# Kernel tuning notes

Measured on AMD Instinct MI355X. Metric: run time of the kernel, lower is better.

## Reference

```python
import jax, jax.numpy as jnp
import numpy as np

HEAD_SIZE = 128  # embeddings_dims // no_of_heads = 4096 // 32


def apply_rope(v):
    # v: [B, S, d] with d = HEAD_SIZE; interleaved-pair rotation as in source
    B, S, d = v.shape
    pos = jnp.arange(S, dtype=jnp.float32)[:, None]              # [S, 1]
    idx = jnp.arange(0, d, 2, dtype=jnp.float32)[None, :]        # [1, d//2]
    theta = jnp.power(10000.0, -2.0 * idx / d)                   # [1, d//2]
    angles = pos * theta                                         # [S, d//2]
    cos = jnp.cos(angles)
    sin = jnp.sin(angles)
    vr = v.reshape(B, S, d // 2, 2)
    x0, x1 = vr[..., 0], vr[..., 1]
    out = jnp.stack([x0 * cos - x1 * sin, x1 * cos + x0 * sin], axis=-1)
    return out.reshape(B, S, d)


def setup_inputs() -> dict:
    key = jax.random.key(0)
    kx, kq, kk, kv = jax.random.split(key, 4)
    B, S, D = 2, 4096, 4096
    d = HEAD_SIZE
    scale = 1.0 / np.sqrt(D)
    return {
        "x": jax.random.normal(kx, (B, S, D), dtype=jnp.float32),
        "Wq": jax.random.normal(kq, (d, D), dtype=jnp.float32) * scale,
        "Wk": jax.random.normal(kk, (d, D), dtype=jnp.float32) * scale,
        "Wv": jax.random.normal(kv, (d, D), dtype=jnp.float32) * scale,
    }


def reference(x, Wq, Wk, Wv):
    # single attention head, non-flash path (eval mode: dropout = identity)
    B, S, D = x.shape
    q = jnp.einsum('bsd,hd->bsh', x, Wq)  # [B, S, head]
    k = jnp.einsum('bsd,hd->bsh', x, Wk)
    v = jnp.einsum('bsd,hd->bsh', x, Wv)
    q = apply_rope(q)
    k = apply_rope(k)
    scale = k.shape[-1] ** (-0.5)
    scores = jnp.einsum('bqh,bkh->bqk', q, k) * scale  # [B, S, S]
    causal = jnp.tril(jnp.ones((S, S), dtype=bool))
    scores = jnp.where(causal, scores, -jnp.inf)
    weights = jax.nn.softmax(scores, axis=-1)
    out = jnp.einsum('bqk,bkh->bqh', weights, v)  # [B, S, head]
    return out
```

## Files before the change

kernel.cpp:

```cpp
#include <hip/hip_runtime.h>

typedef _Float16 half8 __attribute__((ext_vector_type(8)));
typedef _Float16 half2v __attribute__((ext_vector_type(2)));
typedef float f32x4 __attribute__((ext_vector_type(4)));

#define S_LEN 4096
#define D_DIM 4096
#define HD 128


__device__ __forceinline__ void gload_lds16(const _Float16* g, _Float16* l) {
    __builtin_amdgcn_global_load_lds(
        (const __attribute__((address_space(1))) unsigned int*)g,
        (__attribute__((address_space(3))) unsigned int*)l, 16, 0, 0);
}

__global__ __launch_bounds__(256) void convw_kernel(const float* __restrict__ wq,
                                                    const float* __restrict__ wk,
                                                    const float* __restrict__ wv,
                                                    _Float16* __restrict__ wh) {
    const int g = blockIdx.x * 256 + threadIdx.x;
    const int p = g >> 16;
    const int off = (g & 65535) * 8;
    const float* src = ((p == 0) ? wq : (p == 1) ? wk : wv) + off;
    float4 v0 = *(const float4*)src;
    float4 v1 = *(const float4*)(src + 4);
    half8 h = { (_Float16)v0.x, (_Float16)v0.y, (_Float16)v0.z, (_Float16)v0.w,
                (_Float16)v1.x, (_Float16)v1.y, (_Float16)v1.z, (_Float16)v1.w };
    *(half8*)&wh[(size_t)p * 524288 + off] = h;
}

__global__ __launch_bounds__(256) void trig_kernel(float* __restrict__ tab) {
    const int g = blockIdx.x * 256 + threadIdx.x;
    const int s = g >> 6, p = g & 63;
    const float theta = exp2f((float)p * -0.4152410118609203f);
    float sn, cn;
    sincosf((float)s * theta, &sn, &cn);
    *(float2*)&tab[g * 2] = (float2){cn, sn};
}

__global__ __launch_bounds__(256, 3) void proj64_kernel(const float* __restrict__ x,
                                                        const _Float16* __restrict__ wh,
                                                        float* __restrict__ P) {
    __shared__ __align__(16) _Float16 smem[24576];
    const int tid = threadIdx.x;
    const int wg = blockIdx.x;
    const int swz = (wg & 7) * 96 + (wg >> 3);
    const int bx = swz % 3;
    const int rest = swz / 3;
    const int ks = rest & 1;
    const int M0 = (rest >> 1) * 64;
    const int lane = tid & 63, wv_ = tid >> 6;
    const int l15 = lane & 15, quad = lane >> 4;

    const int arow = tid >> 2, acol = (tid & 3) * 16;
    const float* xa = x + (size_t)(M0 + arow) * D_DIM + acol + ks * (D_DIM / 2);
    const int c8a = (tid & 3) * 2;
    const int awoff0 = (((arow >> 4) * 2 + (c8a >> 2)) * 64 + (arow & 15) + (c8a & 3) * 16) * 8;
    const int c8b = c8a + 1;
    const int awoff1 = (((arow >> 4) * 2 + (c8b >> 2)) * 64 + (arow & 15) + (c8b & 3) * 16) * 8;

    const _Float16* wsrc = wh + (size_t)bx * 524288 + ks * (D_DIM / 2) +
                           (size_t)(wv_ * 32 + l15) * D_DIM + quad * 8;

    f32x4 acc[4][2];
    for (int mi = 0; mi < 4; ++mi)
        for (int ni = 0; ni < 2; ++ni)
            acc[mi][ni] = (f32x4){0.f, 0.f, 0.f, 0.f};

    auto stageA = [&](_Float16* buf, float4 A0, float4 A1, float4 A2, float4 A3) {
        half8 h0 = { (_Float16)A0.x, (_Float16)A0.y, (_Float16)A0.z, (_Float16)A0.w,
                     (_Float16)A1.x, (_Float16)A1.y, (_Float16)A1.z, (_Float16)A1.w };
        half8 h1 = { (_Float16)A2.x, (_Float16)A2.y, (_Float16)A2.z, (_Float16)A2.w,
                     (_Float16)A3.x, (_Float16)A3.y, (_Float16)A3.z, (_Float16)A3.w };
        *(half8*)&buf[awoff0] = h0;
        *(half8*)&buf[awoff1] = h1;
    };
    auto stageB = [&](_Float16* buf, int p) {
        const _Float16* s = wsrc + p * 64;
        gload_lds16(s,                     &buf[4096 + ((wv_ * 2 + 0) * 2 + 0) * 512]);
        gload_lds16(s + 32,                &buf[4096 + ((wv_ * 2 + 0) * 2 + 1) * 512]);
        gload_lds16(s + 16 * D_DIM,        &buf[4096 + ((wv_ * 2 + 1) * 2 + 0) * 512]);
        gload_lds16(s + 16 * D_DIM + 32,   &buf[4096 + ((wv_ * 2 + 1) * 2 + 1) * 512]);
    };
    auto compute = [&](const _Float16* buf) {
        const _Float16* Af = buf + lane * 8;
        const _Float16* Bf = buf + 4096 + wv_ * 2048 + lane * 8;
        half8 af[4][2], bf[2][2];
        for (int mi = 0; mi < 4; ++mi)
            for (int kk = 0; kk < 2; ++kk)
                af[mi][kk] = *(const half8*)(Af + (mi * 2 + kk) * 512);
        for (int ni = 0; ni < 2; ++ni)
            for (int kk = 0; kk < 2; ++kk)
                bf[ni][kk] = *(const half8*)(Bf + (ni * 2 + kk) * 512);
        for (int kk = 0; kk < 2; ++kk)
            for (int mi = 0; mi < 4; ++mi)
                for (int ni = 0; ni < 2; ++ni)
                    acc[mi][ni] = __builtin_amdgcn_mfma_f32_16x16x32_f16(af[mi][kk], bf[ni][kk],
                                                                         acc[mi][ni], 0, 0, 0);
    };

#define LOADA(R0, R1, R2, R3, p)                           \
    R0 = *(const float4*)(xa + (p) * 64);                  \
    R1 = *(const float4*)(xa + (p) * 64 + 4);              \
    R2 = *(const float4*)(xa + (p) * 64 + 8);              \
    R3 = *(const float4*)(xa + (p) * 64 + 12);

    float4 aA0, aA1, aA2, aA3, aB0, aB1, aB2, aB3;
    LOADA(aA0, aA1, aA2, aA3, 0)
    LOADA(aB0, aB1, aB2, aB3, 1)
    stageB(smem, 0);

    for (int p = 0; p < 32; p += 2) {
        stageA(smem, aA0, aA1, aA2, aA3);
        __syncthreads();
        if (p + 2 < 32) { LOADA(aA0, aA1, aA2, aA3, p + 2) }
        stageB(smem + 12288, p + 1);
        compute(smem);
        stageA(smem + 12288, aB0, aB1, aB2, aB3);
        __syncthreads();
        if (p + 3 < 32) { LOADA(aB0, aB1, aB2, aB3, p + 3) }
        if (p + 2 < 32) stageB(smem, p + 2);
        compute(smem + 12288);
    }
#undef LOADA
    __syncthreads();

    float* sf = (float*)smem;
    for (int mi = 0; mi < 4; ++mi)
        for (int ni = 0; ni < 2; ++ni)
            for (int r = 0; r < 4; ++r)
                sf[(mi * 16 + quad * 4 + r) * 132 + wv_ * 32 + ni * 16 + l15] =
                    acc[mi][ni][r];
    __syncthreads();
    const int row = tid >> 2, c0 = (tid & 3) * 32;
    float* dst = P + ((size_t)(ks * 3 + bx) * 8192 + M0 + row) * HD + c0;
    for (int j = 0; j < 8; ++j)
        *(float4*)(dst + j * 4) = *(const float4*)&sf[row * 132 + c0 + j * 4];
}

#define QSTR 136
__global__ __launch_bounds__(256) void proj_kernel(const float* __restrict__ x,
                                                   const _Float16* __restrict__ wh,
                                                   _Float16* __restrict__ qw,
                                                   _Float16* __restrict__ kw,
                                                   _Float16* __restrict__ vt) {
    __shared__ __align__(16) _Float16 smem[17408];
    const int tid = threadIdx.x;
    const int wg = blockIdx.x;
    const int swz = (wg & 7) * 48 + (wg >> 3);
    const int bx = swz % 3;
    const int M0 = (swz / 3) * 64;
    const int lane = tid & 63, wv_ = tid >> 6;
    const int l15 = lane & 15, quad = lane >> 4;

    const int arow = tid >> 2, acol = (tid & 3) * 8;
    const float* xa = x + (size_t)(M0 + arow) * D_DIM + acol;
    const _Float16* wsrc = wh + (size_t)bx * 128 * D_DIM +
                           (size_t)(wv_ * 32 + l15) * D_DIM + quad * 8;
    const int awoff = ((arow >> 4) * 64 + (arow & 15) + (tid & 3) * 16) * 8;
    const int rdoff = lane * 8;

    f32x4 acc[4][2];
    for (int mi = 0; mi < 4; ++mi)
        for (int ni = 0; ni < 2; ++ni)
            acc[mi][ni] = (f32x4){0.f, 0.f, 0.f, 0.f};

    auto stageA = [&](_Float16* buf, float4 A0, float4 A1) {
        half8 ha = { (_Float16)A0.x, (_Float16)A0.y, (_Float16)A0.z, (_Float16)A0.w,
                     (_Float16)A1.x, (_Float16)A1.y, (_Float16)A1.z, (_Float16)A1.w };
        *(half8*)&buf[awoff] = ha;
    };
    auto stageB = [&](_Float16* buf, int slab) {
        const _Float16* s = wsrc + slab * 32;
        gload_lds16(s,              &buf[2048 + wv_ * 1024]);
        gload_lds16(s + 16 * D_DIM, &buf[2048 + wv_ * 1024 + 512]);
    };
    auto compute = [&](const _Float16* buf) {
        const _Float16* Af = buf + rdoff;
        const _Float16* Bf = buf + 2048 + wv_ * 1024 + rdoff;
        half8 af[4], bf[2];
        for (int mi = 0; mi < 4; ++mi)
            af[mi] = *(const half8*)(Af + mi * 512);
        for (int ni = 0; ni < 2; ++ni)
            bf[ni] = *(const half8*)(Bf + ni * 512);
        for (int mi = 0; mi < 4; ++mi)
            for (int ni = 0; ni < 2; ++ni)
                acc[mi][ni] = __builtin_amdgcn_mfma_f32_16x16x32_f16(af[mi], bf[ni],
                                                                     acc[mi][ni], 0, 0, 0);
    };

    float4 a0_0, a0_1, a1_0, a1_1;
    a0_0 = *(const float4*)(xa);      a0_1 = *(const float4*)(xa + 4);
    a1_0 = *(const float4*)(xa + 32); a1_1 = *(const float4*)(xa + 36);
    stageB(smem, 0);

    for (int i = 0; i < 128; i += 2) {
        stageA(smem, a0_0, a0_1);
        __syncthreads();
        if (i + 2 < 128) {
            a0_0 = *(const float4*)(xa + (i + 2) * 32);
            a0_1 = *(const float4*)(xa + (i + 2) * 32 + 4);
        }
        stageB(smem + 6144, i + 1);
        compute(smem);
        stageA(smem + 6144, a1_0, a1_1);
        __syncthreads();
        if (i + 3 < 128) {
            a1_0 = *(const float4*)(xa + (i + 3) * 32);
            a1_1 = *(const float4*)(xa + (i + 3) * 32 + 4);
        }
        if (i + 2 < 128) stageB(smem, i + 2);
        compute(smem + 6144);
    }
    __syncthreads();

    if (bx < 2) {
        for (int mi = 0; mi < 4; ++mi)
            for (int ni = 0; ni < 2; ++ni)
                for (int r = 0; r < 4; ++r)
                    smem[(mi * 16 + quad * 4 + r) * QSTR + wv_ * 32 + ni * 16 + l15] =
                        (_Float16)acc[mi][ni][r];
        __syncthreads();
        _Float16* dst = ((bx == 0) ? qw : kw) + (size_t)M0 * HD;
        const int row = tid >> 2, c0 = (tid & 3) * 32;
        for (int j = 0; j < 4; ++j)
            *(half8*)&dst[row * HD + c0 + j * 8] = *(const half8*)&smem[row * QSTR + c0 + j * 8];
    } else {
        for (int mi = 0; mi < 4; ++mi)
            for (int ni = 0; ni < 2; ++ni)
                for (int r = 0; r < 4; ++r)
                    smem[(wv_ * 32 + ni * 16 + l15) * QSTR + mi * 16 + quad * 4 + r] =
                        (_Float16)acc[mi][ni][r];
        __syncthreads();
        _Float16* dst = vt + (size_t)(M0 >> 12) * HD * S_LEN + (M0 & (S_LEN - 1));
        const int hd = tid >> 1, s0 = (tid & 1) * 32;
        for (int j = 0; j < 4; ++j)
            *(half8*)&dst[(size_t)hd * S_LEN + s0 + j * 8] =
                *(const half8*)&smem[hd * QSTR + s0 + j * 8];
    }
}

__global__ __launch_bounds__(256) void combine_kernel(const float* __restrict__ P,
                                                      const float* __restrict__ tab,
                                                      _Float16* __restrict__ qw,
                                                      _Float16* __restrict__ kw,
                                                      _Float16* __restrict__ vt) {
    const int tid = threadIdx.x;
    const int M0 = blockIdx.x * 64;
    const int row = tid >> 2, c0 = (tid & 3) * 32;
    if (blockIdx.y == 0) {
        const float* Pq0 = P + ((size_t)0 * 8192 + M0 + row) * HD + c0;
        const float* Pq1 = P + ((size_t)3 * 8192 + M0 + row) * HD + c0;
        const float* Pk0 = P + ((size_t)1 * 8192 + M0 + row) * HD + c0;
        const float* Pk1 = P + ((size_t)4 * 8192 + M0 + row) * HD + c0;
        float qv[32], kv[32];
#pragma unroll
        for (int j = 0; j < 8; ++j) {
            float4 a = *(const float4*)(Pq0 + j * 4);
            float4 b = *(const float4*)(Pq1 + j * 4);
            float4 c = *(const float4*)(Pk0 + j * 4);
            float4 d = *(const float4*)(Pk1 + j * 4);
            qv[j * 4 + 0] = a.x + b.x; qv[j * 4 + 1] = a.y + b.y;
            qv[j * 4 + 2] = a.z + b.z; qv[j * 4 + 3] = a.w + b.w;
            kv[j * 4 + 0] = c.x + d.x; kv[j * 4 + 1] = c.y + d.y;
            kv[j * 4 + 2] = c.z + d.z; kv[j * 4 + 3] = c.w + d.w;
        }
        const int s = (M0 + row) & (S_LEN - 1);
        const float2* tb = (const float2*)tab + s * 64 + (c0 >> 1);
        half8 oq[4], ok[4];
#pragma unroll
        for (int jp = 0; jp < 16; ++jp) {
            const float2 cs = tb[jp];
            const float cn = cs.x, sn = cs.y;
            const float q0 = qv[2 * jp], q1 = qv[2 * jp + 1];
            const float k0 = kv[2 * jp], k1 = kv[2 * jp + 1];
            oq[jp >> 2][(2 * jp) & 7]     = (_Float16)(q0 * cn - q1 * sn);
            oq[jp >> 2][(2 * jp + 1) & 7] = (_Float16)(q1 * cn + q0 * sn);
            ok[jp >> 2][(2 * jp) & 7]     = (_Float16)(k0 * cn - k1 * sn);
            ok[jp >> 2][(2 * jp + 1) & 7] = (_Float16)(k1 * cn + k0 * sn);
        }
        _Float16* qdst = qw + (size_t)(M0 + row) * HD + c0;
        _Float16* kdst = kw + (size_t)(M0 + row) * HD + c0;
#pragma unroll
        for (int j = 0; j < 4; ++j) {
            *(half8*)(qdst + j * 8) = oq[j];
            *(half8*)(kdst + j * 8) = ok[j];
        }
    } else {
        __shared__ __align__(16) _Float16 sh[128][72];
        const float* Pv0 = P + ((size_t)2 * 8192 + M0 + row) * HD + c0;
        const float* Pv1 = P + ((size_t)5 * 8192 + M0 + row) * HD + c0;
#pragma unroll
        for (int j = 0; j < 8; ++j) {
            float4 a = *(const float4*)(Pv0 + j * 4);
            float4 b = *(const float4*)(Pv1 + j * 4);
            sh[c0 + j * 4 + 0][row] = (_Float16)(a.x + b.x);
            sh[c0 + j * 4 + 1][row] = (_Float16)(a.y + b.y);
            sh[c0 + j * 4 + 2][row] = (_Float16)(a.z + b.z);
            sh[c0 + j * 4 + 3][row] = (_Float16)(a.w + b.w);
        }
        __syncthreads();
        const int hd = tid >> 1, s0 = (tid & 1) * 32;
        _Float16* dst = vt + (size_t)(M0 >> 12) * HD * S_LEN + (size_t)hd * S_LEN +
                        (M0 & (S_LEN - 1)) + s0;
        for (int j = 0; j < 4; ++j)
            *(half8*)(dst + j * 8) = *(const half8*)&sh[hd][s0 + j * 8];
    }
}

__global__ __launch_bounds__(256) void rope_kernel(_Float16* __restrict__ qw,
                                                   _Float16* __restrict__ kw) {
    const int g = blockIdx.x * 256 + threadIdx.x;
    const int m = g >> 6, p = g & 63;
    const int s = m & (S_LEN - 1);
    const float theta = exp2f((float)p * -0.4152410118609203f);
    float sn, cn;
    sincosf((float)s * theta, &sn, &cn);
    const size_t off = (size_t)m * HD + 2 * p;
    half2v qv = *(half2v*)&qw[off];
    half2v kv = *(half2v*)&kw[off];
    float q0 = qv[0], q1 = qv[1], k0 = kv[0], k1 = kv[1];
    half2v qo = { (_Float16)(q0 * cn - q1 * sn), (_Float16)(q1 * cn + q0 * sn) };
    half2v ko = { (_Float16)(k0 * cn - k1 * sn), (_Float16)(k1 * cn + k0 * sn) };
    *(half2v*)&qw[off] = qo;
    *(half2v*)&kw[off] = ko;
}

__device__ __forceinline__ void load_kf(const _Float16* __restrict__ kb, int kbase,
                                        int l15, int quad, half8* kf) {
    const _Float16* kr = kb + (size_t)(kbase + l15) * HD + quad * 8;
    for (int kk = 0; kk < 4; ++kk) {
        kf[kk]     = *(const half8*)(kr + kk * 32);
        kf[4 + kk] = *(const half8*)(kr + 16 * HD + kk * 32);
    }
}

template<bool MASKED>
__device__ __forceinline__ void attn_tile(int kbase, int qg, int l15, int quad,
                                          const half8* kf,
                                          const _Float16* __restrict__ vtb,
                                          const half8* bq, f32x4* acc,
                                          float& mrun, float& lrun) {
    const float csc = 0.1275174348796053f;
    half8 va[8];
    const _Float16* vr = vtb + (size_t)l15 * S_LEN + kbase + quad * 8;
    for (int c = 0; c < 8; ++c)
        va[c] = *(const half8*)(vr + (size_t)c * 16 * S_LEN);
    f32x4 st0 = (f32x4){0.f, 0.f, 0.f, 0.f};
    f32x4 st1 = (f32x4){0.f, 0.f, 0.f, 0.f};
    for (int kk = 0; kk < 4; ++kk) {
        st0 = __builtin_amdgcn_mfma_f32_16x16x32_f16(kf[kk],     bq[kk], st0, 0, 0, 0);
        st1 = __builtin_amdgcn_mfma_f32_16x16x32_f16(kf[4 + kk], bq[kk], st1, 0, 0, 0);
    }
    float p0[4], p1[4];
    float mloc = -1e30f;
    for (int r = 0; r < 4; ++r) {
        float v0 = st0[r] * csc;
        float v1 = st1[r] * csc;
        if (MASKED) {
            const int key0 = kbase + quad * 4 + r;
            if (key0 > qg)      v0 = -1e30f;
            if (key0 + 16 > qg) v1 = -1e30f;
        }
        p0[r] = v0; p1[r] = v1;
        mloc = fmaxf(mloc, fmaxf(v0, v1));
    }
    mloc = fmaxf(mloc, __shfl_xor(mloc, 16));
    mloc = fmaxf(mloc, __shfl_xor(mloc, 32));
    const float mnew = fmaxf(mrun, mloc);
    const float alpha = exp2f(mrun - mnew);
    mrun = mnew;
    float ls = 0.f;
    for (int r = 0; r < 4; ++r) {
        p0[r] = exp2f(p0[r] - mnew);
        p1[r] = exp2f(p1[r] - mnew);
        ls += p0[r] + p1[r];
    }
    ls += __shfl_xor(ls, 16);
    ls += __shfl_xor(ls, 32);
    lrun = lrun * alpha + ls;
    for (int c = 0; c < 8; ++c)
        acc[c] *= alpha;
    int ph0 = __builtin_bit_cast(int, __builtin_amdgcn_cvt_pkrtz(p0[0], p0[1]));
    int ph1 = __builtin_bit_cast(int, __builtin_amdgcn_cvt_pkrtz(p0[2], p0[3]));
    int ph2 = __builtin_bit_cast(int, __builtin_amdgcn_cvt_pkrtz(p1[0], p1[1]));
    int ph3 = __builtin_bit_cast(int, __builtin_amdgcn_cvt_pkrtz(p1[2], p1[3]));
    const int s0 = (l15 + (((quad << 1)    ) & 3) * 16) * 4;
    const int s1 = (l15 + (((quad << 1) + 1) & 3) * 16) * 4;
    int a0 = __builtin_amdgcn_ds_bpermute(s0, ph0);
    int a1 = __builtin_amdgcn_ds_bpermute(s0, ph1);
    int a2 = __builtin_amdgcn_ds_bpermute(s1, ph0);
    int a3 = __builtin_amdgcn_ds_bpermute(s1, ph1);
    int b0 = __builtin_amdgcn_ds_bpermute(s0, ph2);
    int b1 = __builtin_amdgcn_ds_bpermute(s0, ph3);
    int b2 = __builtin_amdgcn_ds_bpermute(s1, ph2);
    int b3 = __builtin_amdgcn_ds_bpermute(s1, ph3);
    const bool lo = quad < 2;
    int4 pi = { lo ? a0 : b0, lo ? a1 : b1, lo ? a2 : b2, lo ? a3 : b3 };
    half8 pf = __builtin_bit_cast(half8, pi);
    for (int c = 0; c < 8; ++c)
        acc[c] = __builtin_amdgcn_mfma_f32_16x16x32_f16(va[c], pf, acc[c], 0, 0, 0);
}

__global__ __launch_bounds__(256) void attn_kernel(const _Float16* __restrict__ q,
                                                   const _Float16* __restrict__ k,
                                                   const _Float16* __restrict__ vt,
                                                   float* __restrict__ out) {
    __shared__ __align__(16) float Osh[4][16][132];
    __shared__ float msh[4][16];
    __shared__ float lsh[4][16];
    const int tid = threadIdx.x;
    const int lane = tid & 63, wv_ = tid >> 6;
    const int l15 = lane & 15, quad = lane >> 4;
    const int bidx = blockIdx.x;
    const int b = bidx & 1;
    const int t = 255 - (bidx >> 1);
    const int qb = t * 16;
    const int qg = qb + l15;

    const _Float16* qp = q + (size_t)(b * S_LEN + qb) * HD;
    half8 bq[4];
    for (int kk = 0; kk < 4; ++kk)
        bq[kk] = *(const half8*)&qp[l15 * HD + kk * 32 + quad * 8];

    f32x4 acc[8];
    for (int c = 0; c < 8; ++c) acc[c] = (f32x4){0.f, 0.f, 0.f, 0.f};
    float mrun = -1e30f, lrun = 0.f;

    const _Float16* kb = k + (size_t)b * S_LEN * HD;
    const _Float16* vtb = vt + (size_t)b * HD * S_LEN;

    const int nfull = (qb + 1) >> 5;
    const int kend = nfull * 32;
    const bool hasm = ((nfull & 3) == wv_);
    const int kb0 = wv_ * 32;

    half8 kf[8], kf2[8];
    if (kb0 < kend)      load_kf(kb, kb0, l15, quad, kf);
    else if (hasm)       load_kf(kb, kend, l15, quad, kf);
    for (int kbase = kb0; kbase < kend; kbase += 128) {
        const int kn = kbase + 128;
        if (kn < kend)   load_kf(kb, kn, l15, quad, kf2);
        else if (hasm)   load_kf(kb, kend, l15, quad, kf2);
        attn_tile<false>(kbase, qg, l15, quad, kf, vtb, bq, acc, mrun, lrun);
        for (int j = 0; j < 8; ++j) kf[j] = kf2[j];
    }
    if (hasm)
        attn_tile<true>(kend, qg, l15, quad, kf, vtb, bq, acc, mrun, lrun);

    for (int c = 0; c < 8; ++c)
        *(f32x4*)&Osh[wv_][l15][c * 16 + quad * 4] = acc[c];
    if (quad == 0) { msh[wv_][l15] = mrun; lsh[wv_][l15] = lrun; }
    __syncthreads();

    const int qr = tid >> 4, dg = (tid & 15) * 8;
    float m0 = msh[0][qr], m1 = msh[1][qr], m2 = msh[2][qr], m3 = msh[3][qr];
    float mm = fmaxf(fmaxf(m0, m1), fmaxf(m2, m3));
    float f0 = exp2f(m0 - mm), f1 = exp2f(m1 - mm), f2 = exp2f(m2 - mm), f3 = exp2f(m3 - mm);
    float l = lsh[0][qr] * f0 + lsh[1][qr] * f1 + lsh[2][qr] * f2 + lsh[3][qr] * f3;
    f32x4 oa = (f32x4){0.f, 0.f, 0.f, 0.f}, ob = oa;
    oa += *(f32x4*)&Osh[0][qr][dg] * f0;  ob += *(f32x4*)&Osh[0][qr][dg + 4] * f0;
    oa += *(f32x4*)&Osh[1][qr][dg] * f1;  ob += *(f32x4*)&Osh[1][qr][dg + 4] * f1;
    oa += *(f32x4*)&Osh[2][qr][dg] * f2;  ob += *(f32x4*)&Osh[2][qr][dg + 4] * f2;
    oa += *(f32x4*)&Osh[3][qr][dg] * f3;  ob += *(f32x4*)&Osh[3][qr][dg + 4] * f3;
    const float inv = 1.0f / l;
    float* op = out + (size_t)(b * S_LEN + qb + qr) * HD + dg;
    *(float4*)op       = (float4){oa[0] * inv, oa[1] * inv, oa[2] * inv, oa[3] * inv};
    *(float4*)(op + 4) = (float4){ob[0] * inv, ob[1] * inv, ob[2] * inv, ob[3] * inv};
}

extern "C" void kernel_launch(void* const* d_in, const int* in_sizes, int n_in,
                              void* d_out, int out_size, void* d_ws, size_t ws_size,
                              hipStream_t stream) {
    const float* x  = (const float*)d_in[0];
    const float* Wq = (const float*)d_in[1];
    const float* Wk = (const float*)d_in[2];
    const float* Wv = (const float*)d_in[3];
    float* out = (float*)d_out;
    char* ws = (char*)d_ws;
    _Float16* qw = (_Float16*)(ws);
    _Float16* kw = (_Float16*)(ws + (2u << 20));
    _Float16* vt = (_Float16*)(ws + (4u << 20));
    _Float16* wh = (_Float16*)(ws + (6u << 20));
    float* P   = (float*)(ws + (9u << 20));
    float* tab = (float*)(ws + (33u << 20));

    const size_t need = (size_t)(35u << 20);
    convw_kernel<<<dim3(768), dim3(256), 0, stream>>>(Wq, Wk, Wv, wh);
    if (ws_size >= need) {
        trig_kernel<<<dim3(1024), dim3(256), 0, stream>>>(tab);
        proj64_kernel<<<dim3(768), dim3(256), 0, stream>>>(x, wh, P);
        combine_kernel<<<dim3(128, 2), dim3(256), 0, stream>>>(P, tab, qw, kw, vt);
    } else {
        proj_kernel<<<dim3(384), dim3(256), 0, stream>>>(x, wh, qw, kw, vt);
        rope_kernel<<<dim3(2048), dim3(256), 0, stream>>>(qw, kw);
    }
    attn_kernel<<<dim3(512), dim3(256), 0, stream>>>(qw, kw, vt, out);
}
```

Before: 349.5 us.

## Process 32 query rows per attention block, fuse setup kernels, drop fallback path

The attention kernel now handles two 16-row query sub-tiles per block. Each K and V tile is loaded once and reused for both, which halves the grid to 256 blocks, and the K double-buffer prefetch is removed. The weight-conversion and trig-table kernels are merged into one launch, and the small-workspace fallback path is deleted. The aim is to cut K/V global traffic and launch overhead, at the cost of more registers, lower occupancy, a smaller grid with coarser causal load balance, and no prefetch overlap.

```diff
diff --git a/kernel.cpp b/kernel.cpp
--- a/kernel.cpp
+++ b/kernel.cpp
@@ -15,28 +15,29 @@
         (__attribute__((address_space(3))) unsigned int*)l, 16, 0, 0);
 }
 
-__global__ __launch_bounds__(256) void convw_kernel(const float* __restrict__ wq,
+__global__ __launch_bounds__(256) void setup_kernel(const float* __restrict__ wq,
                                                     const float* __restrict__ wk,
                                                     const float* __restrict__ wv,
-                                                    _Float16* __restrict__ wh) {
+                                                    _Float16* __restrict__ wh,
+                                                    float* __restrict__ tab) {
     const int g = blockIdx.x * 256 + threadIdx.x;
-    const int p = g >> 16;
-    const int off = (g & 65535) * 8;
-    const float* src = ((p == 0) ? wq : (p == 1) ? wk : wv) + off;
-    float4 v0 = *(const float4*)src;
-    float4 v1 = *(const float4*)(src + 4);
-    half8 h = { (_Float16)v0.x, (_Float16)v0.y, (_Float16)v0.z, (_Float16)v0.w,
-                (_Float16)v1.x, (_Float16)v1.y, (_Float16)v1.z, (_Float16)v1.w };
-    *(half8*)&wh[(size_t)p * 524288 + off] = h;
-}
-
-__global__ __launch_bounds__(256) void trig_kernel(float* __restrict__ tab) {
-    const int g = blockIdx.x * 256 + threadIdx.x;
-    const int s = g >> 6, p = g & 63;
-    const float theta = exp2f((float)p * -0.4152410118609203f);
-    float sn, cn;
-    sincosf((float)s * theta, &sn, &cn);
-    *(float2*)&tab[g * 2] = (float2){cn, sn};
+    if (g < 196608) {
+        const int p = g >> 16;
+        const int off = (g & 65535) * 8;
+        const float* src = ((p == 0) ? wq : (p == 1) ? wk : wv) + off;
+        float4 v0 = *(const float4*)src;
+        float4 v1 = *(const float4*)(src + 4);
+        half8 h = { (_Float16)v0.x, (_Float16)v0.y, (_Float16)v0.z, (_Float16)v0.w,
+                    (_Float16)v1.x, (_Float16)v1.y, (_Float16)v1.z, (_Float16)v1.w };
+        *(half8*)&wh[(size_t)p * 524288 + off] = h;
+    } else {
+        const int h = g - 196608;
+        const int s = h >> 6, p = h & 63;
+        const float theta = exp2f((float)p * -0.4152410118609203f);
+        float sn, cn;
+        sincosf((float)s * theta, &sn, &cn);
+        *(float2*)&tab[h * 2] = (float2){cn, sn};
+    }
 }
 
 __global__ __launch_bounds__(256, 3) void proj64_kernel(const float* __restrict__ x,
@@ -78,10 +79,10 @@
     };
     auto stageB = [&](_Float16* buf, int p) {
         const _Float16* s = wsrc + p * 64;
-        gload_lds16(s,                     &buf[4096 + ((wv_ * 2 + 0) * 2 + 0) * 512]);
-        gload_lds16(s + 32,                &buf[4096 + ((wv_ * 2 + 0) * 2 + 1) * 512]);
-        gload_lds16(s + 16 * D_DIM,        &buf[4096 + ((wv_ * 2 + 1) * 2 + 0) * 512]);
-        gload_lds16(s + 16 * D_DIM + 32,   &buf[4096 + ((wv_ * 2 + 1) * 2 + 1) * 512]);
+        gload_lds16(s,                   &buf[4096 + ((wv_ * 2 + 0) * 2 + 0) * 512]);
+        gload_lds16(s + 32,              &buf[4096 + ((wv_ * 2 + 0) * 2 + 1) * 512]);
+        gload_lds16(s + 16 * D_DIM,      &buf[4096 + ((wv_ * 2 + 1) * 2 + 0) * 512]);
+        gload_lds16(s + 16 * D_DIM + 32, &buf[4096 + ((wv_ * 2 + 1) * 2 + 1) * 512]);
     };
     auto compute = [&](const _Float16* buf) {
         const _Float16* Af = buf + lane * 8;
@@ -137,108 +138,6 @@
     float* dst = P + ((size_t)(ks * 3 + bx) * 8192 + M0 + row) * HD + c0;
     for (int j = 0; j < 8; ++j)
         *(float4*)(dst + j * 4) = *(const float4*)&sf[row * 132 + c0 + j * 4];
-}
-
-#define QSTR 136
-__global__ __launch_bounds__(256) void proj_kernel(const float* __restrict__ x,
-                                                   const _Float16* __restrict__ wh,
-                                                   _Float16* __restrict__ qw,
-                                                   _Float16* __restrict__ kw,
-                                                   _Float16* __restrict__ vt) {
-    __shared__ __align__(16) _Float16 smem[17408];
-    const int tid = threadIdx.x;
-    const int wg = blockIdx.x;
-    const int swz = (wg & 7) * 48 + (wg >> 3);
-    const int bx = swz % 3;
-    const int M0 = (swz / 3) * 64;
-    const int lane = tid & 63, wv_ = tid >> 6;
-    const int l15 = lane & 15, quad = lane >> 4;
-
-    const int arow = tid >> 2, acol = (tid & 3) * 8;
-    const float* xa = x + (size_t)(M0 + arow) * D_DIM + acol;
-    const _Float16* wsrc = wh + (size_t)bx * 128 * D_DIM +
-                           (size_t)(wv_ * 32 + l15) * D_DIM + quad * 8;
-    const int awoff = ((arow >> 4) * 64 + (arow & 15) + (tid & 3) * 16) * 8;
-    const int rdoff = lane * 8;
-
-    f32x4 acc[4][2];
-    for (int mi = 0; mi < 4; ++mi)
-        for (int ni = 0; ni < 2; ++ni)
-            acc[mi][ni] = (f32x4){0.f, 0.f, 0.f, 0.f};
-
-    auto stageA = [&](_Float16* buf, float4 A0, float4 A1) {
-        half8 ha = { (_Float16)A0.x, (_Float16)A0.y, (_Float16)A0.z, (_Float16)A0.w,
-                     (_Float16)A1.x, (_Float16)A1.y, (_Float16)A1.z, (_Float16)A1.w };
-        *(half8*)&buf[awoff] = ha;
-    };
-    auto stageB = [&](_Float16* buf, int slab) {
-        const _Float16* s = wsrc + slab * 32;
-        gload_lds16(s,              &buf[2048 + wv_ * 1024]);
-        gload_lds16(s + 16 * D_DIM, &buf[2048 + wv_ * 1024 + 512]);
-    };
-    auto compute = [&](const _Float16* buf) {
-        const _Float16* Af = buf + rdoff;
-        const _Float16* Bf = buf + 2048 + wv_ * 1024 + rdoff;
-        half8 af[4], bf[2];
-        for (int mi = 0; mi < 4; ++mi)
-            af[mi] = *(const half8*)(Af + mi * 512);
-        for (int ni = 0; ni < 2; ++ni)
-            bf[ni] = *(const half8*)(Bf + ni * 512);
-        for (int mi = 0; mi < 4; ++mi)
-            for (int ni = 0; ni < 2; ++ni)
-                acc[mi][ni] = __builtin_amdgcn_mfma_f32_16x16x32_f16(af[mi], bf[ni],
-                                                                     acc[mi][ni], 0, 0, 0);
-    };
-
-    float4 a0_0, a0_1, a1_0, a1_1;
-    a0_0 = *(const float4*)(xa);      a0_1 = *(const float4*)(xa + 4);
-    a1_0 = *(const float4*)(xa + 32); a1_1 = *(const float4*)(xa + 36);
-    stageB(smem, 0);
-
-    for (int i = 0; i < 128; i += 2) {
-        stageA(smem, a0_0, a0_1);
-        __syncthreads();
-        if (i + 2 < 128) {
-            a0_0 = *(const float4*)(xa + (i + 2) * 32);
-            a0_1 = *(const float4*)(xa + (i + 2) * 32 + 4);
-        }
-        stageB(smem + 6144, i + 1);
-        compute(smem);
-        stageA(smem + 6144, a1_0, a1_1);
-        __syncthreads();
-        if (i + 3 < 128) {
-            a1_0 = *(const float4*)(xa + (i + 3) * 32);
-            a1_1 = *(const float4*)(xa + (i + 3) * 32 + 4);
-        }
-        if (i + 2 < 128) stageB(smem, i + 2);
-        compute(smem + 6144);
-    }
-    __syncthreads();
-
-    if (bx < 2) {
-        for (int mi = 0; mi < 4; ++mi)
-            for (int ni = 0; ni < 2; ++ni)
-                for (int r = 0; r < 4; ++r)
-                    smem[(mi * 16 + quad * 4 + r) * QSTR + wv_ * 32 + ni * 16 + l15] =
-                        (_Float16)acc[mi][ni][r];
-        __syncthreads();
-        _Float16* dst = ((bx == 0) ? qw : kw) + (size_t)M0 * HD;
-        const int row = tid >> 2, c0 = (tid & 3) * 32;
-        for (int j = 0; j < 4; ++j)
-            *(half8*)&dst[row * HD + c0 + j * 8] = *(const half8*)&smem[row * QSTR + c0 + j * 8];
-    } else {
-        for (int mi = 0; mi < 4; ++mi)
-            for (int ni = 0; ni < 2; ++ni)
-                for (int r = 0; r < 4; ++r)
-                    smem[(wv_ * 32 + ni * 16 + l15) * QSTR + mi * 16 + quad * 4 + r] =
-                        (_Float16)acc[mi][ni][r];
-        __syncthreads();
-        _Float16* dst = vt + (size_t)(M0 >> 12) * HD * S_LEN + (M0 & (S_LEN - 1));
-        const int hd = tid >> 1, s0 = (tid & 1) * 32;
-        for (int j = 0; j < 4; ++j)
-            *(half8*)&dst[(size_t)hd * S_LEN + s0 + j * 8] =
-                *(const half8*)&smem[hd * QSTR + s0 + j * 8];
-    }
 }
 
 __global__ __launch_bounds__(256) void combine_kernel(const float* __restrict__ P,
@@ -309,24 +208,6 @@
     }
 }
 
-__global__ __launch_bounds__(256) void rope_kernel(_Float16* __restrict__ qw,
-                                                   _Float16* __restrict__ kw) {
-    const int g = blockIdx.x * 256 + threadIdx.x;
-    const int m = g >> 6, p = g & 63;
-    const int s = m & (S_LEN - 1);
-    const float theta = exp2f((float)p * -0.4152410118609203f);
-    float sn, cn;
-    sincosf((float)s * theta, &sn, &cn);
-    const size_t off = (size_t)m * HD + 2 * p;
-    half2v qv = *(half2v*)&qw[off];
-    half2v kv = *(half2v*)&kw[off];
-    float q0 = qv[0], q1 = qv[1], k0 = kv[0], k1 = kv[1];
-    half2v qo = { (_Float16)(q0 * cn - q1 * sn), (_Float16)(q1 * cn + q0 * sn) };
-    half2v ko = { (_Float16)(k0 * cn - k1 * sn), (_Float16)(k1 * cn + k0 * sn) };
-    *(half2v*)&qw[off] = qo;
-    *(half2v*)&kw[off] = ko;
-}
-
 __device__ __forceinline__ void load_kf(const _Float16* __restrict__ kb, int kbase,
                                         int l15, int quad, half8* kf) {
     const _Float16* kr = kb + (size_t)(kbase + l15) * HD + quad * 8;
@@ -336,17 +217,19 @@
     }
 }
 
-template<bool MASKED>
-__device__ __forceinline__ void attn_tile(int kbase, int qg, int l15, int quad,
-                                          const half8* kf,
-                                          const _Float16* __restrict__ vtb,
-                                          const half8* bq, f32x4* acc,
-                                          float& mrun, float& lrun) {
-    const float csc = 0.1275174348796053f;
-    half8 va[8];
+__device__ __forceinline__ void load_vf(const _Float16* __restrict__ vtb, int kbase,
+                                        int l15, int quad, half8* va) {
     const _Float16* vr = vtb + (size_t)l15 * S_LEN + kbase + quad * 8;
     for (int c = 0; c < 8; ++c)
         va[c] = *(const half8*)(vr + (size_t)c * 16 * S_LEN);
+}
+
+template<bool MASKED>
+__device__ __forceinline__ void attn_sub(int kbase, int qg, int l15, int quad,
+                                         const half8* kf, const half8* va,
+                                         const half8* bq, f32x4* acc,
+                                         float& mrun, float& lrun) {
+    const float csc = 0.1275174348796053f;
     f32x4 st0 = (f32x4){0.f, 0.f, 0.f, 0.f};
     f32x4 st1 = (f32x4){0.f, 0.f, 0.f, 0.f};
     for (int kk = 0; kk < 4; ++kk) {
@@ -415,59 +298,72 @@
     const int l15 = lane & 15, quad = lane >> 4;
     const int bidx = blockIdx.x;
     const int b = bidx & 1;
-    const int t = 255 - (bidx >> 1);
-    const int qb = t * 16;
-    const int qg = qb + l15;
+    const int t = 127 - (bidx >> 1);
+    const int qb = t * 32;
 
     const _Float16* qp = q + (size_t)(b * S_LEN + qb) * HD;
-    half8 bq[4];
-    for (int kk = 0; kk < 4; ++kk)
-        bq[kk] = *(const half8*)&qp[l15 * HD + kk * 32 + quad * 8];
-
-    f32x4 acc[8];
-    for (int c = 0; c < 8; ++c) acc[c] = (f32x4){0.f, 0.f, 0.f, 0.f};
-    float mrun = -1e30f, lrun = 0.f;
+    half8 bq0[4], bq1[4];
+    for (int kk = 0; kk < 4; ++kk) {
+        bq0[kk] = *(const half8*)&qp[l15 * HD + kk * 32 + quad * 8];
+        bq1[kk] = *(const half8*)&qp[(16 + l15) * HD + kk * 32 + quad * 8];
+    }
+
+    f32x4 acc0[8], acc1[8];
+    for (int c = 0; c < 8; ++c) {
+        acc0[c] = (f32x4){0.f, 0.f, 0.f, 0.f};
+        acc1[c] = (f32x4){0.f, 0.f, 0.f, 0.f};
+    }
+    float m0 = -1e30f, l0 = 0.f, m1 = -1e30f, l1 = 0.f;
 
     const _Float16* kb = k + (size_t)b * S_LEN * HD;
     const _Float16* vtb = vt + (size_t)b * HD * S_LEN;
 
-    const int nfull = (qb + 1) >> 5;
-    const int kend = nfull * 32;
+    const int nfull = t;
+    const int kend = qb;
     const bool hasm = ((nfull & 3) == wv_);
     const int kb0 = wv_ * 32;
 
-    half8 kf[8], kf2[8];
-    if (kb0 < kend)      load_kf(kb, kb0, l15, quad, kf);
-    else if (hasm)       load_kf(kb, kend, l15, quad, kf);
+    half8 kf[8], va[8];
     for (int kbase = kb0; kbase < kend; kbase += 128) {
-        const int kn = kbase + 128;
-        if (kn < kend)   load_kf(kb, kn, l15, quad, kf2);
-        else if (hasm)   load_kf(kb, kend, l15, quad, kf2);
-        attn_tile<false>(kbase, qg, l15, quad, kf, vtb, bq, acc, mrun, lrun);
-        for (int j = 0; j < 8; ++j) kf[j] = kf2[j];
-    }
-    if (hasm)
-        attn_tile<true>(kend, qg, l15, quad, kf, vtb, bq, acc, mrun, lrun);
-
-    for (int c = 0; c < 8; ++c)
-        *(f32x4*)&Osh[wv_][l15][c * 16 + quad * 4] = acc[c];
-    if (quad == 0) { msh[wv_][l15] = mrun; lsh[wv_][l15] = lrun; }
-    __syncthreads();
-
-    const int qr = tid >> 4, dg = (tid & 15) * 8;
-    float m0 = msh[0][qr], m1 = msh[1][qr], m2 = msh[2][qr], m3 = msh[3][qr];
-    float mm = fmaxf(fmaxf(m0, m1), fmaxf(m2, m3));
-    float f0 = exp2f(m0 - mm), f1 = exp2f(m1 - mm), f2 = exp2f(m2 - mm), f3 = exp2f(m3 - mm);
-    float l = lsh[0][qr] * f0 + lsh[1][qr] * f1 + lsh[2][qr] * f2 + lsh[3][qr] * f3;
-    f32x4 oa = (f32x4){0.f, 0.f, 0.f, 0.f}, ob = oa;
-    oa += *(f32x4*)&Osh[0][qr][dg] * f0;  ob += *(f32x4*)&Osh[0][qr][dg + 4] * f0;
-    oa += *(f32x4*)&Osh[1][qr][dg] * f1;  ob += *(f32x4*)&Osh[1][qr][dg + 4] * f1;
-    oa += *(f32x4*)&Osh[2][qr][dg] * f2;  ob += *(f32x4*)&Osh[2][qr][dg + 4] * f2;
-    oa += *(f32x4*)&Osh[3][qr][dg] * f3;  ob += *(f32x4*)&Osh[3][qr][dg + 4] * f3;
-    const float inv = 1.0f / l;
-    float* op = out + (size_t)(b * S_LEN + qb + qr) * HD + dg;
-    *(float4*)op       = (float4){oa[0] * inv, oa[1] * inv, oa[2] * inv, oa[3] * inv};
-    *(float4*)(op + 4) = (float4){ob[0] * inv, ob[1] * inv, ob[2] * inv, ob[3] * inv};
+        load_kf(kb, kbase, l15, quad, kf);
+        load_vf(vtb, kbase, l15, quad, va);
+        attn_sub<false>(kbase, qb + l15,      l15, quad, kf, va, bq0, acc0, m0, l0);
+        attn_sub<false>(kbase, qb + 16 + l15, l15, quad, kf, va, bq1, acc1, m1, l1);
+    }
+    if (hasm) {
+        load_kf(kb, kend, l15, quad, kf);
+        load_vf(vtb, kend, l15, quad, va);
+        attn_sub<true>(kend, qb + l15,      l15, quad, kf, va, bq0, acc0, m0, l0);
+        attn_sub<true>(kend, qb + 16 + l15, l15, quad, kf, va, bq1, acc1, m1, l1);
+    }
+
+    for (int s = 0; s < 2; ++s) {
+        if (s) __syncthreads();
+        const f32x4* accs = s ? acc1 : acc0;
+        for (int c = 0; c < 8; ++c)
+            *(f32x4*)&Osh[wv_][l15][c * 16 + quad * 4] = accs[c];
+        if (quad == 0) {
+            msh[wv_][l15] = s ? m1 : m0;
+            lsh[wv_][l15] = s ? l1 : l0;
+        }
+        __syncthreads();
+
+        const int qr = tid >> 4, dg = (tid & 15) * 8;
+        float w0 = msh[0][qr], w1 = msh[1][qr], w2 = msh[2][qr], w3 = msh[3][qr];
+        float mm = fmaxf(fmaxf(w0, w1), fmaxf(w2, w3));
+        float f0 = exp2f(w0 - mm), f1 = exp2f(w1 - mm);
+        float f2 = exp2f(w2 - mm), f3 = exp2f(w3 - mm);
+        float l = lsh[0][qr] * f0 + lsh[1][qr] * f1 + lsh[2][qr] * f2 + lsh[3][qr] * f3;
+        f32x4 oa = (f32x4){0.f, 0.f, 0.f, 0.f}, ob = oa;
+        oa += *(f32x4*)&Osh[0][qr][dg] * f0;  ob += *(f32x4*)&Osh[0][qr][dg + 4] * f0;
+        oa += *(f32x4*)&Osh[1][qr][dg] * f1;  ob += *(f32x4*)&Osh[1][qr][dg + 4] * f1;
+        oa += *(f32x4*)&Osh[2][qr][dg] * f2;  ob += *(f32x4*)&Osh[2][qr][dg + 4] * f2;
+        oa += *(f32x4*)&Osh[3][qr][dg] * f3;  ob += *(f32x4*)&Osh[3][qr][dg + 4] * f3;
+        const float inv = 1.0f / l;
+        float* op = out + (size_t)(b * S_LEN + qb + s * 16 + qr) * HD + dg;
+        *(float4*)op       = (float4){oa[0] * inv, oa[1] * inv, oa[2] * inv, oa[3] * inv};
+        *(float4*)(op + 4) = (float4){ob[0] * inv, ob[1] * inv, ob[2] * inv, ob[3] * inv};
+    }
 }
 
 extern "C" void kernel_launch(void* const* d_in, const int* in_sizes, int n_in,
@@ -486,15 +382,8 @@
     float* P   = (float*)(ws + (9u << 20));
     float* tab = (float*)(ws + (33u << 20));
 
-    const size_t need = (size_t)(35u << 20);
-    convw_kernel<<<dim3(768), dim3(256), 0, stream>>>(Wq, Wk, Wv, wh);
-    if (ws_size >= need) {
-        trig_kernel<<<dim3(1024), dim3(256), 0, stream>>>(tab);
-        proj64_kernel<<<dim3(768), dim3(256), 0, stream>>>(x, wh, P);
-        combine_kernel<<<dim3(128, 2), dim3(256), 0, stream>>>(P, tab, qw, kw, vt);
-    } else {
-        proj_kernel<<<dim3(384), dim3(256), 0, stream>>>(x, wh, qw, kw, vt);
-        rope_kernel<<<dim3(2048), dim3(256), 0, stream>>>(qw, kw);
-    }
-    attn_kernel<<<dim3(512), dim3(256), 0, stream>>>(qw, kw, vt, out);
-}
+    setup_kernel<<<dim3(1792), dim3(256), 0, stream>>>(Wq, Wk, Wv, wh, tab);
+    proj64_kernel<<<dim3(768), dim3(256), 0, stream>>>(x, wh, P);
+    combine_kernel<<<dim3(128, 2), dim3(256), 0, stream>>>(P, tab, qw, kw, vt);
+    attn_kernel<<<dim3(256), dim3(256), 0, stream>>>(qw, kw, vt, out);
+}
```

Measured after the change: 322.6 us. 1.08x faster.
